# Kernel optimization log

Measured on AMD Instinct MI355X. Metric: run time of the kernel, lower is better.

Reference implementation:

```python
import jax, jax.numpy as jnp
import numpy as np

N_NODES = 50000
N_EDGES = 800000
IN_DIM = 128
HID = 64
OUT_DIM = 128
N_GRAPHS = 256


def setup_inputs() -> dict:
    key = jax.random.key(0)
    ks = jax.random.split(key, 8)
    x = jax.random.normal(ks[0], (N_NODES, IN_DIM), dtype=jnp.float32)
    edge_index = jax.random.randint(ks[1], (2, N_EDGES), 0, N_NODES, dtype=jnp.int64)
    batch = jnp.sort(jax.random.randint(ks[2], (N_NODES,), 0, N_GRAPHS, dtype=jnp.int64))
    # Glorot-ish init for GCN weights, zero bias (PyG default bias=True)
    W1 = jax.random.normal(ks[3], (IN_DIM, HID), dtype=jnp.float32) / np.sqrt(IN_DIM)
    b1 = jnp.zeros((HID,), dtype=jnp.float32)
    W2 = jax.random.normal(ks[4], (HID, HID), dtype=jnp.float32) / np.sqrt(HID)
    b2 = jnp.zeros((HID,), dtype=jnp.float32)
    W3 = jax.random.normal(ks[5], (HID, OUT_DIM), dtype=jnp.float32) / np.sqrt(HID)
    b3 = jnp.zeros((OUT_DIM,), dtype=jnp.float32)
    return {"x": x, "edge_index": edge_index, "batch": batch, "num_graphs": N_GRAPHS,
            "W1": W1, "b1": b1, "W2": W2, "b2": b2, "W3": W3, "b3": b3}


def _gcn_norm(edge_index, n_nodes):
    # PyG GCNConv default: add self-loops, symmetric D^{-1/2}(A+I)D^{-1/2} norm.
    loops = jnp.arange(n_nodes, dtype=edge_index.dtype)
    src = jnp.concatenate([edge_index[0], loops])  # [E + N]
    dst = jnp.concatenate([edge_index[1], loops])
    deg = jax.ops.segment_sum(jnp.ones_like(dst, dtype=jnp.float32), dst,
                              num_segments=n_nodes)
    dinv = jnp.where(deg > 0, jax.lax.rsqrt(jnp.maximum(deg, 1.0)), 0.0)
    norm = dinv[src] * dinv[dst]  # [E + N]
    return src, dst, norm


def _gcn_conv(x, W, b, src, dst, norm, n_nodes):
    h = x @ W                                  # [N, F_out] dense GEMM
    msg = h[src] * norm[:, None]               # gather + scale  [E+N, F_out]
    agg = jax.ops.segment_sum(msg, dst, num_segments=n_nodes)
    return agg + b


def reference(x, edge_index, batch, num_graphs, W1, b1, W2, b2, W3, b3):
    n_nodes = x.shape[0]
    src, dst, norm = _gcn_norm(edge_index, n_nodes)
    h = jax.nn.gelu(_gcn_conv(x, W1, b1, src, dst, norm, n_nodes))
    h = jax.nn.gelu(_gcn_conv(h, W2, b2, src, dst, norm, n_nodes))
    h = _gcn_conv(h, W3, b3, src, dst, norm, n_nodes)
    # global_mean_pool over batch segment ids
    sums = jax.ops.segment_sum(h, batch, num_segments=num_graphs)
    counts = jax.ops.segment_sum(jnp.ones((n_nodes,), dtype=h.dtype), batch,
                                 num_segments=num_graphs)
    return sums / jnp.maximum(counts, 1.0)[:, None]
```

## Files before the change

kernel.cpp:

```cpp
#include <hip/hip_runtime.h>
#include <hip/hip_fp16.h>
#include <math.h>

#define N_NODES   50000
#define N_EDGES   800000
#define IN_DIM    128
#define HID       64
#define OUT_DIM   128
#define N_GRAPHS  256
#define MAX_DEG   64
#define PARTS     8
#define PSIZE     (N_NODES / PARTS)
#define EPB       4096
#define AGG_NPB   32

typedef _Float16 half8 __attribute__((ext_vector_type(8)));
typedef float floatx4 __attribute__((ext_vector_type(4)));


__global__ __launch_bounds__(256) void k_build(const int* __restrict__ src,
                                               const int* __restrict__ dst,
                                               int* __restrict__ deg, int* __restrict__ col) {
    int p     = blockIdx.x & (PARTS - 1);
    int chunk = blockIdx.x >> 3;
    int base  = chunk * EPB;
    int lo = p * PSIZE, hi = lo + PSIZE;
#pragma unroll
    for (int j = 0; j < EPB / 256; j++) {
        int e = base + j * 256 + threadIdx.x;
        if (e < N_EDGES) {
            int d = dst[e];
            if (d >= lo && d < hi) {
                int pos = atomicAdd(&deg[d], 1);
                if (pos < MAX_DEG) col[d * MAX_DEG + pos] = src[e];
            }
        }
    }
}

__global__ __launch_bounds__(256) void k_prep(const int* __restrict__ deg,
                                              float* __restrict__ dinv,
                                              const float* __restrict__ W1, __half* __restrict__ Wt1,
                                              const float* __restrict__ W2, __half* __restrict__ Wt2) {
    int blk = blockIdx.x;
    if (blk < 196) {
        int n = blk * 256 + threadIdx.x;
        if (n < N_NODES) dinv[n] = rsqrtf((float)(deg[n] + 1));
    } else if (blk < 200) {
        int idx = (blk - 196) * 256 + threadIdx.x;
        int g = idx >> 6, n = idx & 63;
#pragma unroll
        for (int i = 0; i < 8; i++)
            Wt1[idx * 8 + i] = __float2half(W1[(8 * g + i) * 64 + n]);
    } else {
        int idx = (blk - 200) * 256 + threadIdx.x;
        if (idx < 512) {
            int g = idx >> 6, n = idx & 63;
#pragma unroll
            for (int i = 0; i < 8; i++)
                Wt2[idx * 8 + i] = __float2half(W2[(8 * g + i) * 64 + n]);
        }
    }
}


__global__ __launch_bounds__(256) void k_mfma1(const float* __restrict__ A,
                                               const float* __restrict__ dinv,
                                               const __half* __restrict__ Bp,
                                               __half* __restrict__ C) {
    constexpr int K = IN_DIM, S = K / 32;
    int wv   = threadIdx.x >> 6;
    int lane = threadIdx.x & 63;
    int quad = lane >> 4, l15 = lane & 15;
    int row0 = blockIdx.x * 64 + wv * 16;
    if (row0 >= N_NODES) return;

    half8 bf[S][4];
#pragma unroll
    for (int s = 0; s < S; s++)
#pragma unroll
        for (int j = 0; j < 4; j++)
            bf[s][j] = *(const half8*)(Bp + ((size_t)((4 * s + quad) * 64 + 16 * j + l15)) * 8);

    floatx4 acc[4];
#pragma unroll
    for (int j = 0; j < 4; j++) acc[j] = 0.f;

    int arow = row0 + l15;
    float dv = dinv[arow];
#pragma unroll
    for (int s = 0; s < S; s++) {
        float4 xa = *(const float4*)(A + (size_t)arow * K + 32 * s + quad * 8);
        float4 xb = *(const float4*)(A + (size_t)arow * K + 32 * s + quad * 8 + 4);
        half8 af;
        af[0] = (_Float16)(xa.x * dv); af[1] = (_Float16)(xa.y * dv);
        af[2] = (_Float16)(xa.z * dv); af[3] = (_Float16)(xa.w * dv);
        af[4] = (_Float16)(xb.x * dv); af[5] = (_Float16)(xb.y * dv);
        af[6] = (_Float16)(xb.z * dv); af[7] = (_Float16)(xb.w * dv);
#pragma unroll
        for (int j = 0; j < 4; j++)
            acc[j] = __builtin_amdgcn_mfma_f32_16x16x32_f16(af, bf[s][j], acc[j], 0, 0, 0);
    }
#pragma unroll
    for (int j = 0; j < 4; j++)
#pragma unroll
        for (int r = 0; r < 4; r++)
            C[(size_t)(row0 + quad * 4 + r) * 64 + 16 * j + l15] = __float2half(acc[j][r]);
}


__global__ __launch_bounds__(256) void k_mfma2(const __half* __restrict__ A,
                                               const __half* __restrict__ Bp,
                                               __half* __restrict__ C) {
    constexpr int K = HID, S = K / 32;
    int wv   = threadIdx.x >> 6;
    int lane = threadIdx.x & 63;
    int quad = lane >> 4, l15 = lane & 15;
    int row0 = blockIdx.x * 64 + wv * 16;
    if (row0 >= N_NODES) return;

    half8 bf[S][4];
#pragma unroll
    for (int s = 0; s < S; s++)
#pragma unroll
        for (int j = 0; j < 4; j++)
            bf[s][j] = *(const half8*)(Bp + ((size_t)((4 * s + quad) * 64 + 16 * j + l15)) * 8);

    floatx4 acc[4];
#pragma unroll
    for (int j = 0; j < 4; j++) acc[j] = 0.f;

    int arow = row0 + l15;
#pragma unroll
    for (int s = 0; s < S; s++) {
        half8 af = *(const half8*)(A + (size_t)arow * K + 32 * s + quad * 8);
#pragma unroll
        for (int j = 0; j < 4; j++)
            acc[j] = __builtin_amdgcn_mfma_f32_16x16x32_f16(af, bf[s][j], acc[j], 0, 0, 0);
    }
#pragma unroll
    for (int j = 0; j < 4; j++)
#pragma unroll
        for (int r = 0; r < 4; r++)
            C[(size_t)(row0 + quad * 4 + r) * 64 + 16 * j + l15] = __float2half(acc[j][r]);
}


__device__ __forceinline__ void add8(float* acc, uint4 v) {
    const __half2* h = (const __half2*)&v;
#pragma unroll
    for (int j = 0; j < 4; j++) {
        acc[2 * j]     += __low2float(h[j]);
        acc[2 * j + 1] += __high2float(h[j]);
    }
}

__global__ __launch_bounds__(256) void k_agg(const __half* __restrict__ T,
                                             const int* __restrict__ col,
                                             const int* __restrict__ indeg,
                                             const float* __restrict__ dinv,
                                             const float* __restrict__ b,
                                             __half* __restrict__ OUT, int mode) {
    __shared__ int cols[AGG_NPB][MAX_DEG + 1];
    int base = blockIdx.x * AGG_NPB;

    for (int idx = threadIdx.x; idx < AGG_NPB * MAX_DEG; idx += 256) {
        int r = idx >> 6, j = idx & 63;
        int g = base + r;
        if (g < N_NODES) cols[r][j] = col[g * MAX_DEG + j];
    }
    __syncthreads();

    int lane = threadIdx.x & 63;
    int wv   = threadIdx.x >> 6;
    int q = lane >> 3, t = lane & 7;
    int local = wv * 8 + q;
    int d = base + local;
    if (d >= N_NODES) return;

    int dg = indeg[d]; if (dg > MAX_DEG) dg = MAX_DEG;

    float acc[8];
#pragma unroll
    for (int j = 0; j < 8; j++) acc[j] = 0.f;
    add8(acc, *(const uint4*)(T + (size_t)d * HID + t * 8));

    const int* cl = cols[local];
    int i = 0;
    for (; i + 4 <= dg; i += 4) {
        int s0 = cl[i], s1 = cl[i + 1], s2 = cl[i + 2], s3 = cl[i + 3];
        uint4 v0 = *(const uint4*)(T + (size_t)s0 * HID + t * 8);
        uint4 v1 = *(const uint4*)(T + (size_t)s1 * HID + t * 8);
        uint4 v2 = *(const uint4*)(T + (size_t)s2 * HID + t * 8);
        uint4 v3 = *(const uint4*)(T + (size_t)s3 * HID + t * 8);
        add8(acc, v0); add8(acc, v1); add8(acc, v2); add8(acc, v3);
    }
    for (; i < dg; i++) {
        int s = cl[i];
        add8(acc, *(const uint4*)(T + (size_t)s * HID + t * 8));
    }

    float dv = dinv[d];
    float o[8];
#pragma unroll
    for (int j = 0; j < 8; j++) o[j] = acc[j] * dv;
    if (mode == 0) {
#pragma unroll
        for (int j = 0; j < 8; j++) {
            float v = o[j] + b[t * 8 + j];
            float u2 = 0.7978845608028654f * (v + 0.044715f * v * v * v);
            o[j] = 0.5f * v * (1.0f + tanhf(u2)) * dv;
        }
    }
    __half2 hh[4];
#pragma unroll
    for (int j = 0; j < 4; j++) hh[j] = __floats2half2_rn(o[2 * j], o[2 * j + 1]);
    *(uint4*)(OUT + (size_t)d * HID + t * 8) = *(uint4*)hh;
}


__global__ __launch_bounds__(256) void k_pool_out(const __half* __restrict__ A,
                                                  const int* __restrict__ batch,
                                                  const float* __restrict__ W3,
                                                  const float* __restrict__ b3,
                                                  float* __restrict__ out) {
    int g = blockIdx.x;
    int lo = 0, hi = N_NODES;
    while (lo < hi) { int m = (lo + hi) >> 1; if (batch[m] < g) lo = m + 1; else hi = m; }
    int lo2 = lo, hi2 = N_NODES;
    while (lo2 < hi2) { int m = (lo2 + hi2) >> 1; if (batch[m] < g + 1) lo2 = m + 1; else hi2 = m; }
    int start = lo, end = lo2;

    int lane = threadIdx.x & 63;
    int wave = threadIdx.x >> 6;
    float acc = 0.f;
    for (int n = start + wave; n < end; n += 4)
        acc += __half2float(A[(size_t)n * HID + lane]);

    __shared__ float part[4][HID];
    __shared__ float pooled[HID];
    part[wave][lane] = acc;
    __syncthreads();
    if (threadIdx.x < HID)
        pooled[threadIdx.x] = part[0][threadIdx.x] + part[1][threadIdx.x] +
                              part[2][threadIdx.x] + part[3][threadIdx.x];
    __syncthreads();

    if (threadIdx.x < OUT_DIM) {
        float cntf = (float)(end - start);
        float inv = 1.0f / fmaxf(cntf, 1.0f);
        float s = 0.f;
#pragma unroll
        for (int k = 0; k < HID; k++) s += pooled[k] * W3[k * OUT_DIM + threadIdx.x];
        out[g * OUT_DIM + threadIdx.x] = (s + cntf * b3[threadIdx.x]) * inv;
    }
}


extern "C" void kernel_launch(void* const* d_in, const int* in_sizes, int n_in,
                              void* d_out, int out_size, void* d_ws, size_t ws_size,
                              hipStream_t stream) {
    const float* x     = (const float*)d_in[0];
    const int*   ei    = (const int*)d_in[1];
    const int*   batch = (const int*)d_in[2];
    const float* W1    = (const float*)d_in[4];
    const float* b1    = (const float*)d_in[5];
    const float* W2    = (const float*)d_in[6];
    const float* b2    = (const float*)d_in[7];
    const float* W3    = (const float*)d_in[8];
    const float* b3    = (const float*)d_in[9];
    float* out = (float*)d_out;

    const int* esrc = ei;
    const int* edst = ei + N_EDGES;

    int*    deg  = (int*)d_ws;
    float*  dinv = (float*)(deg + N_NODES);
    int*    col  = (int*)(dinv + N_NODES);
    __half* t    = (__half*)(col + (size_t)N_NODES * MAX_DEG);
    __half* p    = t + (size_t)N_NODES * HID;
    __half* Wt1  = p + (size_t)N_NODES * HID;
    __half* Wt2  = Wt1 + IN_DIM * HID;

    hipMemsetAsync(deg, 0, (size_t)N_NODES * 4, stream);

    const int CHUNKS = (N_EDGES + EPB - 1) / EPB;
    k_build<<<CHUNKS * PARTS, 256, 0, stream>>>(esrc, edst, deg, col);
    k_prep<<<202, 256, 0, stream>>>(deg, dinv, W1, Wt1, W2, Wt2);

    const int GB = (N_NODES + 63) / 64;
    const int AB = (N_NODES + AGG_NPB - 1) / AGG_NPB;

    k_mfma1<<<GB, 256, 0, stream>>>(x, dinv, Wt1, t);
    k_agg<<<AB, 256, 0, stream>>>(t, col, deg, dinv, b1, p, 0);
    k_mfma2<<<GB, 256, 0, stream>>>(p, Wt2, t);
    k_agg<<<AB, 256, 0, stream>>>(t, col, deg, dinv, b2, p, 0);
    k_agg<<<AB, 256, 0, stream>>>(p, col, deg, dinv, b3, t, 1);
    k_pool_out<<<N_GRAPHS, 256, 0, stream>>>(t, batch, W3, b3, out);
}
```

Baseline: 214.2 us.

## Split feature tables into two column halves and aggregate each half separately

Intermediate node feature tables are stored as two separate 32-column halves, and each aggregation layer runs as two launches, one per half. The goal is a smaller gather working set per pass (1.6M halves per table) so random neighbor reads hit cache more often. The cost is reading the column lists and degrees twice and twice the launches. Nontemporal loads and stores are also added for streaming data, and AGG_NPB is doubled so each block covers 64 nodes with 4 lanes per node.

```diff
diff --git a/kernel.cpp b/kernel.cpp
--- a/kernel.cpp
+++ b/kernel.cpp
@@ -6,16 +6,19 @@
 #define N_EDGES   800000
 #define IN_DIM    128
 #define HID       64
+#define HALF_F    32
+#define TBL       ((size_t)N_NODES * HALF_F)
 #define OUT_DIM   128
 #define N_GRAPHS  256
 #define MAX_DEG   64
 #define PARTS     8
 #define PSIZE     (N_NODES / PARTS)
 #define EPB       4096
-#define AGG_NPB   32
+#define AGG_NPB   64
 
 typedef _Float16 half8 __attribute__((ext_vector_type(8)));
 typedef float floatx4 __attribute__((ext_vector_type(4)));
+typedef unsigned int uintx4 __attribute__((ext_vector_type(4)));
 
 
 __global__ __launch_bounds__(256) void k_build(const int* __restrict__ src,
@@ -63,6 +66,10 @@
     }
 }
 
+__device__ __forceinline__ void store_split(__half* C, int row, int f, float v) {
+    C[(size_t)(f >> 5) * TBL + (size_t)row * HALF_F + (f & 31)] = __float2half(v);
+}
+
 
 __global__ __launch_bounds__(256) void k_mfma1(const float* __restrict__ A,
                                                const float* __restrict__ dinv,
@@ -90,13 +97,13 @@
     float dv = dinv[arow];
 #pragma unroll
     for (int s = 0; s < S; s++) {
-        float4 xa = *(const float4*)(A + (size_t)arow * K + 32 * s + quad * 8);
-        float4 xb = *(const float4*)(A + (size_t)arow * K + 32 * s + quad * 8 + 4);
+        floatx4 xa = __builtin_nontemporal_load((const floatx4*)(A + (size_t)arow * K + 32 * s + quad * 8));
+        floatx4 xb = __builtin_nontemporal_load((const floatx4*)(A + (size_t)arow * K + 32 * s + quad * 8 + 4));
         half8 af;
-        af[0] = (_Float16)(xa.x * dv); af[1] = (_Float16)(xa.y * dv);
-        af[2] = (_Float16)(xa.z * dv); af[3] = (_Float16)(xa.w * dv);
-        af[4] = (_Float16)(xb.x * dv); af[5] = (_Float16)(xb.y * dv);
-        af[6] = (_Float16)(xb.z * dv); af[7] = (_Float16)(xb.w * dv);
+        af[0] = (_Float16)(xa[0] * dv); af[1] = (_Float16)(xa[1] * dv);
+        af[2] = (_Float16)(xa[2] * dv); af[3] = (_Float16)(xa[3] * dv);
+        af[4] = (_Float16)(xb[0] * dv); af[5] = (_Float16)(xb[1] * dv);
+        af[6] = (_Float16)(xb[2] * dv); af[7] = (_Float16)(xb[3] * dv);
 #pragma unroll
         for (int j = 0; j < 4; j++)
             acc[j] = __builtin_amdgcn_mfma_f32_16x16x32_f16(af, bf[s][j], acc[j], 0, 0, 0);
@@ -105,14 +112,14 @@
     for (int j = 0; j < 4; j++)
 #pragma unroll
         for (int r = 0; r < 4; r++)
-            C[(size_t)(row0 + quad * 4 + r) * 64 + 16 * j + l15] = __float2half(acc[j][r]);
+            store_split(C, row0 + quad * 4 + r, 16 * j + l15, acc[j][r]);
 }
 
 
 __global__ __launch_bounds__(256) void k_mfma2(const __half* __restrict__ A,
                                                const __half* __restrict__ Bp,
                                                __half* __restrict__ C) {
-    constexpr int K = HID, S = K / 32;
+    constexpr int S = 2;
     int wv   = threadIdx.x >> 6;
     int lane = threadIdx.x & 63;
     int quad = lane >> 4, l15 = lane & 15;
@@ -133,7 +140,7 @@
     int arow = row0 + l15;
 #pragma unroll
     for (int s = 0; s < S; s++) {
-        half8 af = *(const half8*)(A + (size_t)arow * K + 32 * s + quad * 8);
+        half8 af = *(const half8*)(A + (size_t)s * TBL + (size_t)arow * HALF_F + quad * 8);
 #pragma unroll
         for (int j = 0; j < 4; j++)
             acc[j] = __builtin_amdgcn_mfma_f32_16x16x32_f16(af, bf[s][j], acc[j], 0, 0, 0);
@@ -142,11 +149,11 @@
     for (int j = 0; j < 4; j++)
 #pragma unroll
         for (int r = 0; r < 4; r++)
-            C[(size_t)(row0 + quad * 4 + r) * 64 + 16 * j + l15] = __float2half(acc[j][r]);
-}
-
-
-__device__ __forceinline__ void add8(float* acc, uint4 v) {
+            store_split(C, row0 + quad * 4 + r, 16 * j + l15, acc[j][r]);
+}
+
+
+__device__ __forceinline__ void add8(float* acc, uintx4 v) {
     const __half2* h = (const __half2*)&v;
 #pragma unroll
     for (int j = 0; j < 4; j++) {
@@ -155,50 +162,52 @@
     }
 }
 
-__global__ __launch_bounds__(256) void k_agg(const __half* __restrict__ T,
+__global__ __launch_bounds__(256) void k_agg(const __half* __restrict__ Tbase,
                                              const int* __restrict__ col,
-                                             const int* __restrict__ indeg,
+                                             const int* __restrict__ deg,
                                              const float* __restrict__ dinv,
                                              const float* __restrict__ b,
-                                             __half* __restrict__ OUT, int mode) {
+                                             __half* __restrict__ OUTbase,
+                                             int h, int mode) {
     __shared__ int cols[AGG_NPB][MAX_DEG + 1];
     int base = blockIdx.x * AGG_NPB;
 
     for (int idx = threadIdx.x; idx < AGG_NPB * MAX_DEG; idx += 256) {
         int r = idx >> 6, j = idx & 63;
         int g = base + r;
-        if (g < N_NODES) cols[r][j] = col[g * MAX_DEG + j];
+        if (g < N_NODES) cols[r][j] = __builtin_nontemporal_load(&col[g * MAX_DEG + j]);
     }
     __syncthreads();
+
+    const __half* T   = Tbase   + (size_t)h * TBL;
+    __half*       OUT = OUTbase + (size_t)h * TBL;
 
     int lane = threadIdx.x & 63;
     int wv   = threadIdx.x >> 6;
-    int q = lane >> 3, t = lane & 7;
-    int local = wv * 8 + q;
+    int q = lane >> 2, t = lane & 3;
+    int local = wv * 16 + q;
     int d = base + local;
     if (d >= N_NODES) return;
 
-    int dg = indeg[d]; if (dg > MAX_DEG) dg = MAX_DEG;
+    int dg = deg[d]; if (dg > MAX_DEG) dg = MAX_DEG;
 
     float acc[8];
 #pragma unroll
     for (int j = 0; j < 8; j++) acc[j] = 0.f;
-    add8(acc, *(const uint4*)(T + (size_t)d * HID + t * 8));
+    add8(acc, *(const uintx4*)(T + (size_t)d * HALF_F + t * 8));
 
     const int* cl = cols[local];
     int i = 0;
     for (; i + 4 <= dg; i += 4) {
         int s0 = cl[i], s1 = cl[i + 1], s2 = cl[i + 2], s3 = cl[i + 3];
-        uint4 v0 = *(const uint4*)(T + (size_t)s0 * HID + t * 8);
-        uint4 v1 = *(const uint4*)(T + (size_t)s1 * HID + t * 8);
-        uint4 v2 = *(const uint4*)(T + (size_t)s2 * HID + t * 8);
-        uint4 v3 = *(const uint4*)(T + (size_t)s3 * HID + t * 8);
+        uintx4 v0 = *(const uintx4*)(T + (size_t)s0 * HALF_F + t * 8);
+        uintx4 v1 = *(const uintx4*)(T + (size_t)s1 * HALF_F + t * 8);
+        uintx4 v2 = *(const uintx4*)(T + (size_t)s2 * HALF_F + t * 8);
+        uintx4 v3 = *(const uintx4*)(T + (size_t)s3 * HALF_F + t * 8);
         add8(acc, v0); add8(acc, v1); add8(acc, v2); add8(acc, v3);
     }
-    for (; i < dg; i++) {
-        int s = cl[i];
-        add8(acc, *(const uint4*)(T + (size_t)s * HID + t * 8));
-    }
+    for (; i < dg; i++)
+        add8(acc, *(const uintx4*)(T + (size_t)cl[i] * HALF_F + t * 8));
 
     float dv = dinv[d];
     float o[8];
@@ -207,7 +216,7 @@
     if (mode == 0) {
 #pragma unroll
         for (int j = 0; j < 8; j++) {
-            float v = o[j] + b[t * 8 + j];
+            float v = o[j] + b[h * HALF_F + t * 8 + j];
             float u2 = 0.7978845608028654f * (v + 0.044715f * v * v * v);
             o[j] = 0.5f * v * (1.0f + tanhf(u2)) * dv;
         }
@@ -215,7 +224,8 @@
     __half2 hh[4];
 #pragma unroll
     for (int j = 0; j < 4; j++) hh[j] = __floats2half2_rn(o[2 * j], o[2 * j + 1]);
-    *(uint4*)(OUT + (size_t)d * HID + t * 8) = *(uint4*)hh;
+    uintx4 st = *(uintx4*)hh;
+    __builtin_nontemporal_store(st, (uintx4*)(OUT + (size_t)d * HALF_F + t * 8));
 }
 
 
@@ -233,9 +243,10 @@
 
     int lane = threadIdx.x & 63;
     int wave = threadIdx.x >> 6;
+    size_t foff = (size_t)(lane >> 5) * TBL + (lane & 31);
     float acc = 0.f;
     for (int n = start + wave; n < end; n += 4)
-        acc += __half2float(A[(size_t)n * HID + lane]);
+        acc += __half2float(A[(size_t)n * HALF_F + foff]);
 
     __shared__ float part[4][HID];
     __shared__ float pooled[HID];
@@ -278,11 +289,11 @@
     float*  dinv = (float*)(deg + N_NODES);
     int*    col  = (int*)(dinv + N_NODES);
     __half* t    = (__half*)(col + (size_t)N_NODES * MAX_DEG);
-    __half* p    = t + (size_t)N_NODES * HID;
-    __half* Wt1  = p + (size_t)N_NODES * HID;
+    __half* p    = t + 2 * TBL;
+    __half* Wt1  = p + 2 * TBL;
     __half* Wt2  = Wt1 + IN_DIM * HID;
 
-    hipMemsetAsync(deg, 0, (size_t)N_NODES * 4, stream);
+    (void)hipMemsetAsync(deg, 0, (size_t)N_NODES * 4, stream);
 
     const int CHUNKS = (N_EDGES + EPB - 1) / EPB;
     k_build<<<CHUNKS * PARTS, 256, 0, stream>>>(esrc, edst, deg, col);
@@ -292,9 +303,12 @@
     const int AB = (N_NODES + AGG_NPB - 1) / AGG_NPB;
 
     k_mfma1<<<GB, 256, 0, stream>>>(x, dinv, Wt1, t);
-    k_agg<<<AB, 256, 0, stream>>>(t, col, deg, dinv, b1, p, 0);
+    k_agg<<<AB, 256, 0, stream>>>(t, col, deg, dinv, b1, p, 0, 0);
+    k_agg<<<AB, 256, 0, stream>>>(t, col, deg, dinv, b1, p, 1, 0);
     k_mfma2<<<GB, 256, 0, stream>>>(p, Wt2, t);
-    k_agg<<<AB, 256, 0, stream>>>(t, col, deg, dinv, b2, p, 0);
-    k_agg<<<AB, 256, 0, stream>>>(p, col, deg, dinv, b3, t, 1);
+    k_agg<<<AB, 256, 0, stream>>>(t, col, deg, dinv, b2, p, 0, 0);
+    k_agg<<<AB, 256, 0, stream>>>(t, col, deg, dinv, b2, p, 1, 0);
+    k_agg<<<AB, 256, 0, stream>>>(p, col, deg, dinv, b3, t, 0, 1);
+    k_agg<<<AB, 256, 0, stream>>>(p, col, deg, dinv, b3, t, 1, 1);
     k_pool_out<<<N_GRAPHS, 256, 0, stream>>>(t, batch, W3, b3, out);
 }
```

New measurement: 282.2 us. 1.32x slower.

## Split each node's neighbor gather across two waves and reduce via shared memory

Applied to the files above, without the earlier changes.

The aggregation kernel now handles 16 nodes per block, with two waves per node group each gathering alternating neighbors before combining partial sums through shared memory. The gather loop is unrolled to 8 loads in flight, and bounds checks are dropped because 50000 is divisible by 16. Nontemporal loads and stores are added for the input features, column lists and outputs. The aim is more memory parallelism and latency hiding in the gather-bound aggregation, at the cost of an extra block-wide barrier and twice as many blocks.

```diff
diff --git a/kernel.cpp b/kernel.cpp
--- a/kernel.cpp
+++ b/kernel.cpp
@@ -12,10 +12,11 @@
 #define PARTS     8
 #define PSIZE     (N_NODES / PARTS)
 #define EPB       4096
-#define AGG_NPB   32
+#define AGG_NPB   16
 
 typedef _Float16 half8 __attribute__((ext_vector_type(8)));
 typedef float floatx4 __attribute__((ext_vector_type(4)));
+typedef unsigned int uintx4 __attribute__((ext_vector_type(4)));
 
 
 __global__ __launch_bounds__(256) void k_build(const int* __restrict__ src,
@@ -90,13 +91,13 @@
     float dv = dinv[arow];
 #pragma unroll
     for (int s = 0; s < S; s++) {
-        float4 xa = *(const float4*)(A + (size_t)arow * K + 32 * s + quad * 8);
-        float4 xb = *(const float4*)(A + (size_t)arow * K + 32 * s + quad * 8 + 4);
+        floatx4 xa = __builtin_nontemporal_load((const floatx4*)(A + (size_t)arow * K + 32 * s + quad * 8));
+        floatx4 xb = __builtin_nontemporal_load((const floatx4*)(A + (size_t)arow * K + 32 * s + quad * 8 + 4));
         half8 af;
-        af[0] = (_Float16)(xa.x * dv); af[1] = (_Float16)(xa.y * dv);
-        af[2] = (_Float16)(xa.z * dv); af[3] = (_Float16)(xa.w * dv);
-        af[4] = (_Float16)(xb.x * dv); af[5] = (_Float16)(xb.y * dv);
-        af[6] = (_Float16)(xb.z * dv); af[7] = (_Float16)(xb.w * dv);
+        af[0] = (_Float16)(xa[0] * dv); af[1] = (_Float16)(xa[1] * dv);
+        af[2] = (_Float16)(xa[2] * dv); af[3] = (_Float16)(xa[3] * dv);
+        af[4] = (_Float16)(xb[0] * dv); af[5] = (_Float16)(xb[1] * dv);
+        af[6] = (_Float16)(xb[2] * dv); af[7] = (_Float16)(xb[3] * dv);
 #pragma unroll
         for (int j = 0; j < 4; j++)
             acc[j] = __builtin_amdgcn_mfma_f32_16x16x32_f16(af, bf[s][j], acc[j], 0, 0, 0);
@@ -112,7 +113,7 @@
 __global__ __launch_bounds__(256) void k_mfma2(const __half* __restrict__ A,
                                                const __half* __restrict__ Bp,
                                                __half* __restrict__ C) {
-    constexpr int K = HID, S = K / 32;
+    constexpr int S = HID / 32;
     int wv   = threadIdx.x >> 6;
     int lane = threadIdx.x & 63;
     int quad = lane >> 4, l15 = lane & 15;
@@ -133,7 +134,7 @@
     int arow = row0 + l15;
 #pragma unroll
     for (int s = 0; s < S; s++) {
-        half8 af = *(const half8*)(A + (size_t)arow * K + 32 * s + quad * 8);
+        half8 af = *(const half8*)(A + (size_t)arow * HID + 32 * s + quad * 8);
 #pragma unroll
         for (int j = 0; j < 4; j++)
             acc[j] = __builtin_amdgcn_mfma_f32_16x16x32_f16(af, bf[s][j], acc[j], 0, 0, 0);
@@ -146,7 +147,7 @@
 }
 
 
-__device__ __forceinline__ void add8(float* acc, uint4 v) {
+__device__ __forceinline__ void add8(float* acc, uintx4 v) {
     const __half2* h = (const __half2*)&v;
 #pragma unroll
     for (int j = 0; j < 4; j++) {
@@ -157,65 +158,81 @@
 
 __global__ __launch_bounds__(256) void k_agg(const __half* __restrict__ T,
                                              const int* __restrict__ col,
-                                             const int* __restrict__ indeg,
+                                             const int* __restrict__ deg,
                                              const float* __restrict__ dinv,
                                              const float* __restrict__ b,
                                              __half* __restrict__ OUT, int mode) {
     __shared__ int cols[AGG_NPB][MAX_DEG + 1];
+    __shared__ float part[2][8][65];
+    int tid = threadIdx.x;
     int base = blockIdx.x * AGG_NPB;
 
-    for (int idx = threadIdx.x; idx < AGG_NPB * MAX_DEG; idx += 256) {
+    for (int idx = tid; idx < AGG_NPB * MAX_DEG; idx += 256) {
         int r = idx >> 6, j = idx & 63;
-        int g = base + r;
-        if (g < N_NODES) cols[r][j] = col[g * MAX_DEG + j];
+        cols[r][j] = __builtin_nontemporal_load(&col[(base + r) * MAX_DEG + j]);
     }
     __syncthreads();
 
-    int lane = threadIdx.x & 63;
-    int wv   = threadIdx.x >> 6;
+    int lane = tid & 63, wv = tid >> 6;
+    int pair = wv >> 1, half = wv & 1;
     int q = lane >> 3, t = lane & 7;
-    int local = wv * 8 + q;
+    int local = pair * 8 + q;
     int d = base + local;
-    if (d >= N_NODES) return;
-
-    int dg = indeg[d]; if (dg > MAX_DEG) dg = MAX_DEG;
+
+    int dg = deg[d]; if (dg > MAX_DEG) dg = MAX_DEG;
+    int cnt = (dg - half + 1) >> 1;
 
     float acc[8];
 #pragma unroll
     for (int j = 0; j < 8; j++) acc[j] = 0.f;
-    add8(acc, *(const uint4*)(T + (size_t)d * HID + t * 8));
+    if (half == 0)
+        add8(acc, *(const uintx4*)(T + (size_t)d * HID + t * 8));
 
     const int* cl = cols[local];
     int i = 0;
-    for (; i + 4 <= dg; i += 4) {
-        int s0 = cl[i], s1 = cl[i + 1], s2 = cl[i + 2], s3 = cl[i + 3];
-        uint4 v0 = *(const uint4*)(T + (size_t)s0 * HID + t * 8);
-        uint4 v1 = *(const uint4*)(T + (size_t)s1 * HID + t * 8);
-        uint4 v2 = *(const uint4*)(T + (size_t)s2 * HID + t * 8);
-        uint4 v3 = *(const uint4*)(T + (size_t)s3 * HID + t * 8);
-        add8(acc, v0); add8(acc, v1); add8(acc, v2); add8(acc, v3);
-    }
-    for (; i < dg; i++) {
-        int s = cl[i];
-        add8(acc, *(const uint4*)(T + (size_t)s * HID + t * 8));
-    }
-
-    float dv = dinv[d];
-    float o[8];
-#pragma unroll
-    for (int j = 0; j < 8; j++) o[j] = acc[j] * dv;
-    if (mode == 0) {
-#pragma unroll
-        for (int j = 0; j < 8; j++) {
-            float v = o[j] + b[t * 8 + j];
-            float u2 = 0.7978845608028654f * (v + 0.044715f * v * v * v);
-            o[j] = 0.5f * v * (1.0f + tanhf(u2)) * dv;
+    for (; i + 8 <= cnt; i += 8) {
+        uintx4 v[8];
+#pragma unroll
+        for (int u = 0; u < 8; u++)
+            v[u] = *(const uintx4*)(T + (size_t)cl[2 * (i + u) + half] * HID + t * 8);
+#pragma unroll
+        for (int u = 0; u < 8; u++) add8(acc, v[u]);
+    }
+    for (; i + 2 <= cnt; i += 2) {
+        uintx4 v0 = *(const uintx4*)(T + (size_t)cl[2 * i + half] * HID + t * 8);
+        uintx4 v1 = *(const uintx4*)(T + (size_t)cl[2 * (i + 1) + half] * HID + t * 8);
+        add8(acc, v0); add8(acc, v1);
+    }
+    if (i < cnt)
+        add8(acc, *(const uintx4*)(T + (size_t)cl[2 * i + half] * HID + t * 8));
+
+    if (half == 1) {
+#pragma unroll
+        for (int j = 0; j < 8; j++) part[pair][q][t * 8 + j] = acc[j];
+    }
+    __syncthreads();
+    if (half == 0) {
+#pragma unroll
+        for (int j = 0; j < 8; j++) acc[j] += part[pair][q][t * 8 + j];
+
+        float dv = dinv[d];
+        float o[8];
+#pragma unroll
+        for (int j = 0; j < 8; j++) o[j] = acc[j] * dv;
+        if (mode == 0) {
+#pragma unroll
+            for (int j = 0; j < 8; j++) {
+                float v = o[j] + b[t * 8 + j];
+                float u2 = 0.7978845608028654f * (v + 0.044715f * v * v * v);
+                o[j] = 0.5f * v * (1.0f + tanhf(u2)) * dv;
+            }
         }
-    }
-    __half2 hh[4];
-#pragma unroll
-    for (int j = 0; j < 4; j++) hh[j] = __floats2half2_rn(o[2 * j], o[2 * j + 1]);
-    *(uint4*)(OUT + (size_t)d * HID + t * 8) = *(uint4*)hh;
+        __half2 hh[4];
+#pragma unroll
+        for (int j = 0; j < 4; j++) hh[j] = __floats2half2_rn(o[2 * j], o[2 * j + 1]);
+        uintx4 st = *(uintx4*)hh;
+        __builtin_nontemporal_store(st, (uintx4*)(OUT + (size_t)d * HID + t * 8));
+    }
 }
 
 
@@ -282,14 +299,14 @@
     __half* Wt1  = p + (size_t)N_NODES * HID;
     __half* Wt2  = Wt1 + IN_DIM * HID;
 
-    hipMemsetAsync(deg, 0, (size_t)N_NODES * 4, stream);
+    (void)hipMemsetAsync(deg, 0, (size_t)N_NODES * 4, stream);
 
     const int CHUNKS = (N_EDGES + EPB - 1) / EPB;
     k_build<<<CHUNKS * PARTS, 256, 0, stream>>>(esrc, edst, deg, col);
     k_prep<<<202, 256, 0, stream>>>(deg, dinv, W1, Wt1, W2, Wt2);
 
     const int GB = (N_NODES + 63) / 64;
-    const int AB = (N_NODES + AGG_NPB - 1) / AGG_NPB;
+    const int AB = N_NODES / AGG_NPB;
 
     k_mfma1<<<GB, 256, 0, stream>>>(x, dinv, Wt1, t);
     k_agg<<<AB, 256, 0, stream>>>(t, col, deg, dinv, b1, p, 0);
```

Result: slower. 245.8 us (+14.7%).
